# Optimization experiments

Measured on AMD Instinct MI355X. Metric: run time of the kernel, lower is better.

## Reference

```python
import jax, jax.numpy as jnp
import numpy as np

NEG = -9e15
SLOPE = 0.02

def setup_inputs() -> dict:
    key = jax.random.key(0)
    k1, k2, k3, k4 = jax.random.split(key, 4)
    N, IN, OUT = 16384, 128, 64
    x = jax.random.normal(k1, (N, IN), dtype=jnp.float32)
    adj = jax.random.randint(k2, (N, N), 0, 2, dtype=jnp.int32)
    weight = jax.random.normal(k3, (IN, OUT), dtype=jnp.float32) * (1.0 / np.sqrt(IN))
    att_weight = jax.random.normal(k4, (2 * OUT, 1), dtype=jnp.float32) * (1.0 / np.sqrt(2 * OUT))
    return {"x": x, "adj": adj, "weight": weight, "att_weight": att_weight}

def reference(x, adj, weight, att_weight):
    out_feature = weight.shape[1]
    Wh = x @ weight                                   # [N, out]
    f_i = Wh @ att_weight[:out_feature, :]            # [N, 1] source term
    f_j = Wh @ att_weight[out_feature:, :]            # [N, 1] dest term
    e = f_i + f_j.T                                   # [N, N] additive scores
    e = jax.nn.leaky_relu(e, negative_slope=SLOPE)
    att = jnp.where(adj > 0, e, NEG)
    att = jax.nn.softmax(att, axis=1)                 # masked row softmax
    h_prime = att @ Wh                                # [N, out]
    return jax.nn.elu(h_prime)                        # concat=True -> elu
```

## Files before the change

### kernel.cpp

```cpp
#include <hip/hip_runtime.h>
#include <cstdint>
#include <cstddef>

#define GN   16384
#define GIN  128
#define GOUT 64
#define NCH  8
#define LOG2E 1.44269504088896340736f

typedef __attribute__((ext_vector_type(8))) short short8;
typedef __attribute__((ext_vector_type(4))) float f32x4;
typedef __attribute__((ext_vector_type(4))) int   int4v;

__device__ __forceinline__ unsigned short f2bf(float f) {
  unsigned u = __float_as_uint(f);
  return (unsigned short)((u + 0x8000u) >> 16);
}

__device__ __forceinline__ unsigned short f2bf_rne(float f) {
  unsigned u = __float_as_uint(f);
  u += 0x7FFFu + ((u >> 16) & 1u);
  return (unsigned short)(u >> 16);
}

__global__ __launch_bounds__(256) void prep_kernel(
    const float* __restrict__ x, const float* __restrict__ w,
    const float* __restrict__ aw, unsigned short* __restrict__ wpk,
    float* __restrict__ fs2, float* __restrict__ fd2)
{
  __shared__ float ws[GIN * GOUT];
  __shared__ float red[2][64][4];

  const int t = threadIdx.x;
  const int rb = blockIdx.x * 64;

  for (int i = t; i < (GIN * GOUT) / 4; i += 256)
    ((float4*)ws)[i] = ((const float4*)w)[i];
  __syncthreads();

  const int r = t & 63, s = t >> 6;
  const int row = rb + r;
  const float* xr = x + (size_t)row * GIN;

  float acc[16];
#pragma unroll
  for (int d = 0; d < 16; ++d) acc[d] = 0.f;

  for (int kk = 0; kk < GIN; kk += 4) {
    float4 xv = *(const float4*)(xr + kk);
    float xa[4] = {xv.x, xv.y, xv.z, xv.w};
#pragma unroll
    for (int u = 0; u < 4; ++u) {
#pragma unroll
      for (int d = 0; d < 16; ++d)
        acc[d] += xa[u] * ws[(kk + u) * GOUT + s * 16 + d];
    }
  }

  const int jc = row >> 5;
  const int qq = (row & 31) >> 3;
  const int tt = row & 7;
  float psrc = 0.f, pdst = 0.f;
#pragma unroll
  for (int d = 0; d < 16; ++d) {
    const int dg = s * 16 + d;
    psrc += acc[d] * aw[dg];
    pdst += acc[d] * aw[GOUT + dg];
    const int f = dg >> 4, n = dg & 15;
    wpk[(size_t)jc * 4096 + f * 1024 + (qq * 16 + n) * 8 + tt] = f2bf_rne(acc[d]);
  }
  red[0][r][s] = psrc;
  red[1][r][s] = pdst;
  __syncthreads();
  if (s == 0) {
    float a_ = red[0][r][0] + red[0][r][1] + red[0][r][2] + red[0][r][3];
    float b_ = red[1][r][0] + red[1][r][1] + red[1][r][2] + red[1][r][3];
    fs2[row] = a_ * LOG2E;
    fd2[row] = b_ * LOG2E;
  }
}

__global__ __launch_bounds__(256) void gat_main(
    const int* __restrict__ adj, const unsigned short* __restrict__ wpk,
    const float* __restrict__ fs2, const float* __restrict__ fd2,
    float* __restrict__ nump, float* __restrict__ denp)
{
  const int wave  = blockIdx.x * 4 + (threadIdx.x >> 6);
  const int lane  = threadIdx.x & 63;
  const int strip = wave & 255;
  const int chunk = wave >> 8;
  const int m = lane & 15;
  const int q = lane >> 4;

  int   row[4];
  float fs[4];
  const int4v* __restrict__ arow[4];
#pragma unroll
  for (int g = 0; g < 4; ++g) {
    row[g] = strip * 64 + g * 16 + m;
    fs[g] = fs2[row[g]];
    arow[g] = (const int4v*)(adj + (size_t)row[g] * GN);
  }

  const int CW = GN / NCH;
  const int j0 = chunk * CW;
  const float4* __restrict__ fdv  = (const float4*)fd2;
  const short8* __restrict__ wpk8 = (const short8*)wpk;

  f32x4 acc[4][4];
  f32x4 accd[4];
#pragma unroll
  for (int g = 0; g < 4; ++g) {
    accd[g] = (f32x4){0.f, 0.f, 0.f, 0.f};
#pragma unroll
    for (int b = 0; b < 4; ++b) acc[g][b] = (f32x4){0.f, 0.f, 0.f, 0.f};
  }

  short8 b_ones;
#pragma unroll
  for (int i = 0; i < 8; ++i) b_ones[i] = (short)0x3F80;

  auto pcalc = [&](int a, float fd, float fsv) -> unsigned short {
    float sv = fsv + fd;
    float lv = fmaxf(sv, 0.02f * sv);
    float pe = __builtin_amdgcn_exp2f(lv);
    pe = (a != 0) ? pe : 0.f;
    return f2bf(pe);
  };

  auto mk_af = [&](int4v aA, int4v aB, float4 fA, float4 fB, float fsv) -> short8 {
    short8 af;
    af[0] = (short)pcalc(aA.x, fA.x, fsv);
    af[1] = (short)pcalc(aA.y, fA.y, fsv);
    af[2] = (short)pcalc(aA.z, fA.z, fsv);
    af[3] = (short)pcalc(aA.w, fA.w, fsv);
    af[4] = (short)pcalc(aB.x, fB.x, fsv);
    af[5] = (short)pcalc(aB.y, fB.y, fsv);
    af[6] = (short)pcalc(aB.z, fB.z, fsv);
    af[7] = (short)pcalc(aB.w, fB.w, fsv);
    return af;
  };

#pragma unroll 1
  for (int j = j0; j < j0 + CW; j += 32) {
    const int i4 = (j >> 2) + (q << 1);

    int4v a0[4], a1[4];
#pragma unroll
    for (int g = 0; g < 4; ++g) {
      a0[g] = __builtin_nontemporal_load(arow[g] + i4);
      a1[g] = __builtin_nontemporal_load(arow[g] + i4 + 1);
    }
    float4 f0 = fdv[i4];
    float4 f1 = fdv[i4 + 1];

    const short8* wb = wpk8 + (size_t)(j >> 5) * 512 + lane;
    short8 b0 = wb[0];
    short8 b1 = wb[128];
    short8 b2 = wb[256];
    short8 b3 = wb[384];

#pragma unroll
    for (int g = 0; g < 4; ++g) {
      short8 af = mk_af(a0[g], a1[g], f0, f1, fs[g]);
      acc[g][0] = __builtin_amdgcn_mfma_f32_16x16x32_bf16(af, b0, acc[g][0], 0, 0, 0);
      acc[g][1] = __builtin_amdgcn_mfma_f32_16x16x32_bf16(af, b1, acc[g][1], 0, 0, 0);
      acc[g][2] = __builtin_amdgcn_mfma_f32_16x16x32_bf16(af, b2, acc[g][2], 0, 0, 0);
      acc[g][3] = __builtin_amdgcn_mfma_f32_16x16x32_bf16(af, b3, acc[g][3], 0, 0, 0);
      accd[g]   = __builtin_amdgcn_mfma_f32_16x16x32_bf16(af, b_ones, accd[g], 0, 0, 0);
    }
  }

  float* np = nump + (size_t)chunk * GN * GOUT;
  float* dp = denp + (size_t)chunk * GN;
#pragma unroll
  for (int g = 0; g < 4; ++g) {
    const int orow0 = strip * 64 + g * 16 + q * 4;
#pragma unroll
    for (int r = 0; r < 4; ++r) {
      float* nr = np + (size_t)(orow0 + r) * GOUT + m;
      __builtin_nontemporal_store(acc[g][0][r], nr + 0);
      __builtin_nontemporal_store(acc[g][1][r], nr + 16);
      __builtin_nontemporal_store(acc[g][2][r], nr + 32);
      __builtin_nontemporal_store(acc[g][3][r], nr + 48);
      if (m == 0) dp[orow0 + r] = accd[g][r];
    }
  }
}

__global__ __launch_bounds__(256) void fin_kernel(
    const float* __restrict__ nump, const float* __restrict__ denp,
    float* __restrict__ out)
{
  const int g = blockIdx.x * 256 + threadIdx.x;
  if (g >= GN * GOUT) return;
  const int row = g >> 6;
  float s = 0.f, d = 0.f;
#pragma unroll
  for (int c = 0; c < NCH; ++c) {
    s += nump[(size_t)c * GN * GOUT + g];
    d += denp[(size_t)c * GN + row];
  }
  float v = s / d;
  out[g] = (v > 0.f) ? v : expm1f(v);
}

extern "C" void kernel_launch(void* const* d_in, const int* in_sizes, int n_in,
                              void* d_out, int out_size, void* d_ws, size_t ws_size,
                              hipStream_t stream) {
  const float* x   = (const float*)d_in[0];
  const int*   adj = (const int*)d_in[1];
  const float* w   = (const float*)d_in[2];
  const float* aw  = (const float*)d_in[3];
  float* out = (float*)d_out;

  float* nump = (float*)d_ws;
  float* denp = nump + (size_t)NCH * GN * GOUT;
  float* fs2  = denp + (size_t)NCH * GN;
  float* fd2  = fs2 + GN;
  unsigned short* wpk = (unsigned short*)(fd2 + GN);

  prep_kernel<<<GN / 64, 256, 0, stream>>>(x, w, aw, wpk, fs2, fd2);
  gat_main<<<(GN / 64) * NCH / 4, 256, 0, stream>>>(adj, wpk, fs2, fd2, nump, denp);
  fin_kernel<<<(GN * GOUT) / 256, 256, 0, stream>>>(nump, denp, out);
}
```

Before: 1.387 ms.

## Pack adjacency into bitmask in separate pass before attention kernel

Adds a mask_kernel that streams the int32 adjacency matrix once and writes one bit per edge. gat_main then reads 32-bit mask words instead of int4 adjacency vectors. The aim is to decouple the bandwidth-bound adjacency read from the MFMA/exp compute loop so the main kernel stays compute-bound. The full adjacency is still read once, so this adds a launch and a small extra write; the benefit depends on the old main loop being stalled on latency rather than on bandwidth.

Result: slower. 1.483 ms (+6.9%).

```diff
diff --git a/kernel.cpp b/kernel.cpp
--- a/kernel.cpp
+++ b/kernel.cpp
@@ -21,6 +21,27 @@
   unsigned u = __float_as_uint(f);
   u += 0x7FFFu + ((u >> 16) & 1u);
   return (unsigned short)(u >> 16);
+}
+
+__global__ __launch_bounds__(256) void mask_kernel(
+    const int* __restrict__ adj, unsigned char* __restrict__ msk)
+{
+  const unsigned nb = (unsigned)((size_t)GN * (size_t)GN / 8);
+  const unsigned stride = gridDim.x * 256;
+  for (unsigned b = blockIdx.x * 256 + threadIdx.x; b < nb; b += stride) {
+    const int4v* p = (const int4v*)(adj + (size_t)b * 8);
+    int4v x0 = __builtin_nontemporal_load(p);
+    int4v x1 = __builtin_nontemporal_load(p + 1);
+    unsigned by = (unsigned)(x0.x != 0)
+                | ((unsigned)(x0.y != 0) << 1)
+                | ((unsigned)(x0.z != 0) << 2)
+                | ((unsigned)(x0.w != 0) << 3)
+                | ((unsigned)(x1.x != 0) << 4)
+                | ((unsigned)(x1.y != 0) << 5)
+                | ((unsigned)(x1.z != 0) << 6)
+                | ((unsigned)(x1.w != 0) << 7);
+    msk[b] = (unsigned char)by;
+  }
 }
 
 __global__ __launch_bounds__(256) void prep_kernel(
@@ -81,7 +102,7 @@
 }
 
 __global__ __launch_bounds__(256) void gat_main(
-    const int* __restrict__ adj, const unsigned short* __restrict__ wpk,
+    const unsigned* __restrict__ bmw, const unsigned short* __restrict__ wpk,
     const float* __restrict__ fs2, const float* __restrict__ fd2,
     float* __restrict__ nump, float* __restrict__ denp)
 {
@@ -91,15 +112,16 @@
   const int chunk = wave >> 8;
   const int m = lane & 15;
   const int q = lane >> 4;
+  const int q8 = q << 3;
 
   int   row[4];
   float fs[4];
-  const int4v* __restrict__ arow[4];
+  const unsigned* __restrict__ bmr[4];
 #pragma unroll
   for (int g = 0; g < 4; ++g) {
     row[g] = strip * 64 + g * 16 + m;
     fs[g] = fs2[row[g]];
-    arow[g] = (const int4v*)(adj + (size_t)row[g] * GN);
+    bmr[g] = bmw + (size_t)row[g] * (GN / 32);
   }
 
   const int CW = GN / NCH;
@@ -120,41 +142,40 @@
 #pragma unroll
   for (int i = 0; i < 8; ++i) b_ones[i] = (short)0x3F80;
 
-  auto pcalc = [&](int a, float fd, float fsv) -> unsigned short {
+  auto pelem = [&](unsigned byte, int t, float fd, float fsv) -> unsigned short {
     float sv = fsv + fd;
     float lv = fmaxf(sv, 0.02f * sv);
     float pe = __builtin_amdgcn_exp2f(lv);
-    pe = (a != 0) ? pe : 0.f;
+    pe = (byte & (1u << t)) ? pe : 0.f;
     return f2bf(pe);
   };
 
-  auto mk_af = [&](int4v aA, int4v aB, float4 fA, float4 fB, float fsv) -> short8 {
+  auto mk_af = [&](unsigned byte, float4 fA, float4 fB, float fsv) -> short8 {
     short8 af;
-    af[0] = (short)pcalc(aA.x, fA.x, fsv);
-    af[1] = (short)pcalc(aA.y, fA.y, fsv);
-    af[2] = (short)pcalc(aA.z, fA.z, fsv);
-    af[3] = (short)pcalc(aA.w, fA.w, fsv);
-    af[4] = (short)pcalc(aB.x, fB.x, fsv);
-    af[5] = (short)pcalc(aB.y, fB.y, fsv);
-    af[6] = (short)pcalc(aB.z, fB.z, fsv);
-    af[7] = (short)pcalc(aB.w, fB.w, fsv);
+    af[0] = (short)pelem(byte, 0, fA.x, fsv);
+    af[1] = (short)pelem(byte, 1, fA.y, fsv);
+    af[2] = (short)pelem(byte, 2, fA.z, fsv);
+    af[3] = (short)pelem(byte, 3, fA.w, fsv);
+    af[4] = (short)pelem(byte, 4, fB.x, fsv);
+    af[5] = (short)pelem(byte, 5, fB.y, fsv);
+    af[6] = (short)pelem(byte, 6, fB.z, fsv);
+    af[7] = (short)pelem(byte, 7, fB.w, fsv);
     return af;
   };
 
 #pragma unroll 1
   for (int j = j0; j < j0 + CW; j += 32) {
     const int i4 = (j >> 2) + (q << 1);
-
-    int4v a0[4], a1[4];
-#pragma unroll
-    for (int g = 0; g < 4; ++g) {
-      a0[g] = __builtin_nontemporal_load(arow[g] + i4);
-      a1[g] = __builtin_nontemporal_load(arow[g] + i4 + 1);
-    }
+    const int wi = j >> 5;
+
+    unsigned wv[4];
+#pragma unroll
+    for (int g = 0; g < 4; ++g) wv[g] = bmr[g][wi];
+
     float4 f0 = fdv[i4];
     float4 f1 = fdv[i4 + 1];
 
-    const short8* wb = wpk8 + (size_t)(j >> 5) * 512 + lane;
+    const short8* wb = wpk8 + (size_t)wi * 512 + lane;
     short8 b0 = wb[0];
     short8 b1 = wb[128];
     short8 b2 = wb[256];
@@ -162,7 +183,8 @@
 
 #pragma unroll
     for (int g = 0; g < 4; ++g) {
-      short8 af = mk_af(a0[g], a1[g], f0, f1, fs[g]);
+      const unsigned byte = (wv[g] >> q8) & 0xffu;
+      short8 af = mk_af(byte, f0, f1, fs[g]);
       acc[g][0] = __builtin_amdgcn_mfma_f32_16x16x32_bf16(af, b0, acc[g][0], 0, 0, 0);
       acc[g][1] = __builtin_amdgcn_mfma_f32_16x16x32_bf16(af, b1, acc[g][1], 0, 0, 0);
       acc[g][2] = __builtin_amdgcn_mfma_f32_16x16x32_bf16(af, b2, acc[g][2], 0, 0, 0);
@@ -219,8 +241,10 @@
   float* fs2  = denp + (size_t)NCH * GN;
   float* fd2  = fs2 + GN;
   unsigned short* wpk = (unsigned short*)(fd2 + GN);
-
+  unsigned char* msk = (unsigned char*)(wpk + (size_t)512 * 4096);
+
+  mask_kernel<<<2048, 256, 0, stream>>>(adj, msk);
   prep_kernel<<<GN / 64, 256, 0, stream>>>(x, w, aw, wpk, fs2, fd2);
-  gat_main<<<(GN / 64) * NCH / 4, 256, 0, stream>>>(adj, wpk, fs2, fd2, nump, denp);
+  gat_main<<<(GN / 64) * NCH / 4, 256, 0, stream>>>((const unsigned*)msk, wpk, fs2, fd2, nump, denp);
   fin_kernel<<<(GN * GOUT) / 256, 256, 0, stream>>>(nump, denp, out);
 }
```
